# Performance work log

Hardware: AMD Instinct MI355X
Metric: run time of the kernel (lower is better)

Reference implementation:

```python
import jax, jax.numpy as jnp
import numpy as np

INPUT_DIM = 512
OUTPUT_DIM = 512
GRID_SIZE = 16
INPUT_MIN = -1.0
INPUT_RANGE = 2.0


def setup_inputs() -> dict:
    key = jax.random.key(0)
    k_x, k_mix = jax.random.split(key)
    x = jax.random.normal(k_x, (65536, INPUT_DIM), dtype=jnp.float32)
    # per-dim spline tables: bases init zeros, slopes init 0.1 (as in torch)
    bases = jnp.zeros((INPUT_DIM, GRID_SIZE), dtype=jnp.float32)
    slopes = jnp.full((INPUT_DIM, GRID_SIZE), 0.1, dtype=jnp.float32)
    mix = jax.random.normal(k_mix, (OUTPUT_DIM, INPUT_DIM), dtype=jnp.float32) * 0.01
    bias = jnp.zeros((OUTPUT_DIM,), dtype=jnp.float32)
    return {"x": x, "bases": bases, "slopes": slopes, "mix": mix, "bias": bias}


def reference(x, bases, slopes, mix, bias):
    # x: [B, D]; bases/slopes: [D, G]; mix: [O, D]; bias: [O]
    B, D = x.shape
    G = bases.shape[1]
    x_norm = jnp.clip((x - INPUT_MIN) / INPUT_RANGE, 0.0, 1.0 - 1e-6)
    idx = jnp.clip((x_norm * G).astype(jnp.int32), 0, G - 1)        # [B, D]
    x_local = x_norm * G - idx.astype(x.dtype)                       # fractional position in cell
    # gather per-dim table entries: flatten [D, G] and index with d*G + idx
    flat_idx = jnp.arange(D, dtype=jnp.int32)[None, :] * G + idx    # [B, D]
    base = bases.reshape(-1)[flat_idx]                               # [B, D]
    slope = slopes.reshape(-1)[flat_idx]                             # [B, D]
    spline_out = base + slope * x_local                              # [B, D]
    y = jnp.einsum('bd,od->bo', spline_out, mix) + bias              # [B, O]
    return y
```

## Files before the change

kernel.cpp:

```cpp
#include <hip/hip_runtime.h>


#define DIMK 512
#define DIMN 512
#define GRID_G 16

typedef unsigned short u16;
typedef unsigned int u32;
typedef __attribute__((ext_vector_type(8))) __bf16 bf16x8;
typedef __attribute__((ext_vector_type(4))) float f32x4;

__device__ __forceinline__ u32 bf16rne(float f) {
    u32 u = __float_as_uint(f);
    return (u + 0x7fffu + ((u >> 16) & 1u)) >> 16;
}

__global__ void prep_kernel(const float* __restrict__ mix,
                            u16* __restrict__ mixb) {
    int t = blockIdx.x * 256 + threadIdx.x;
    float4 v = reinterpret_cast<const float4*>(mix)[t];
    ushort4 o;
    o.x = (u16)bf16rne(v.x);
    o.y = (u16)bf16rne(v.y);
    o.z = (u16)bf16rne(v.z);
    o.w = (u16)bf16rne(v.w);
    reinterpret_cast<ushort4*>(mixb)[t] = o;
}

__global__ __launch_bounds__(512, 2) void kan_kernel(
    const float* __restrict__ x, const float* __restrict__ bases,
    const float* __restrict__ slopes, const u16* __restrict__ mixb,
    const float* __restrict__ bias, float* __restrict__ y) {
    __shared__ u32 s_tab[DIMK * 17];
    __shared__ __align__(16) u16 sA[128 * 32];
    __shared__ __align__(16) u16 sB[512 * 32];

    const int tid = threadIdx.x;
    const int lane = tid & 63;
    const int wid = tid >> 6;
    const int quad = lane >> 4;
    const int l15 = lane & 15;
    const int wave_m = wid >> 2;
    const int wave_n = wid & 3;
    const int m0 = blockIdx.x * 128;

#pragma unroll
    for (int k = 0; k < 16; k++) {
        int i = tid + k * 512;
        u32 p = bf16rne(bases[i]) | (bf16rne(slopes[i]) << 16);
        s_tab[(i >> 4) * 17 + (i & 15)] = p;
    }

    const int ar = tid >> 2;
    const int akg = tid & 3;
    const int awchunk = (ar << 2) | (akg ^ ((ar >> 1) & 3));
    const float4* xrow =
        reinterpret_cast<const float4*>(x + (size_t)(m0 + ar) * DIMK) + akg * 2;

    f32x4 acc[4][8];
#pragma unroll
    for (int i = 0; i < 4; i++)
#pragma unroll
        for (int j = 0; j < 8; j++) acc[i][j] = (f32x4){0.f, 0.f, 0.f, 0.f};

    float4 xa = xrow[0];
    float4 xb = xrow[1];

    __syncthreads();

    for (int kt = 0; kt < 16; ++kt) {
        float xs[8] = {xa.x, xa.y, xa.z, xa.w, xb.x, xb.y, xb.z, xb.w};
        const int dbase = kt * 32 + akg * 8;
        u32 h[8];
#pragma unroll
        for (int j = 0; j < 8; j++) {
            float xn = fminf(fmaxf((xs[j] + 1.0f) * 0.5f, 0.0f), 0.999999f);
            float tt = xn * 16.0f;
            int idx = (int)tt;
            u32 p = s_tab[(dbase + j) * 17 + idx];
            float base = __uint_as_float(p << 16);
            float slope = __uint_as_float(p & 0xffff0000u);
            float sp = fmaf(slope, tt - (float)idx, base);
            h[j] = bf16rne(sp);
        }
        int4 pk = make_int4((int)(h[0] | (h[1] << 16)), (int)(h[2] | (h[3] << 16)),
                            (int)(h[4] | (h[5] << 16)), (int)(h[6] | (h[7] << 16)));
        *reinterpret_cast<int4*>(&sA[awchunk * 8]) = pk;

#pragma unroll
        for (int i = 0; i < 4; i++) {
            int grp = wid * 4 + i;
            int n = grp * 16 + (lane >> 2);
            int c = (lane & 3) ^ ((n >> 1) & 3);
            const u16* gsrc = mixb + (size_t)n * DIMK + kt * 32 + c * 8;
            __builtin_amdgcn_global_load_lds(
                (const __attribute__((address_space(1))) void*)gsrc,
                (__attribute__((address_space(3))) void*)(&sB[grp * 512]),
                16, 0, 0);
        }
        __syncthreads();

        if (kt < 15) {
            xa = xrow[(kt + 1) * 8];
            xb = xrow[(kt + 1) * 8 + 1];
        }

        bf16x8 afrag[4];
#pragma unroll
        for (int fm = 0; fm < 4; fm++) {
            int m_l = wave_m * 64 + fm * 16 + l15;
            int ci = (m_l << 2) | (quad ^ ((m_l >> 1) & 3));
            afrag[fm] = *reinterpret_cast<const bf16x8*>(&sA[ci * 8]);
        }
#pragma unroll
        for (int fn = 0; fn < 8; fn++) {
            int n_l = wave_n * 128 + fn * 16 + l15;
            int ci = (n_l << 2) | (quad ^ ((n_l >> 1) & 3));
            bf16x8 bfrag = *reinterpret_cast<const bf16x8*>(&sB[ci * 8]);
#pragma unroll
            for (int fm = 0; fm < 4; fm++)
                acc[fm][fn] = __builtin_amdgcn_mfma_f32_16x16x32_bf16(
                    afrag[fm], bfrag, acc[fm][fn], 0, 0, 0);
        }
        __syncthreads();
    }

#pragma unroll
    for (int fn = 0; fn < 8; fn++) {
        int o = wave_n * 128 + fn * 16 + l15;
        float bv = bias[o];
#pragma unroll
        for (int fm = 0; fm < 4; fm++) {
            int row = m0 + wave_m * 64 + fm * 16 + quad * 4;
            float* yp = y + (size_t)row * DIMN + o;
#pragma unroll
            for (int j = 0; j < 4; j++)
                yp[(size_t)j * DIMN] = acc[fm][fn][j] + bv;
        }
    }
}

extern "C" void kernel_launch(void* const* d_in, const int* in_sizes, int n_in,
                              void* d_out, int out_size, void* d_ws, size_t ws_size,
                              hipStream_t stream) {
    const float* x = (const float*)d_in[0];
    const float* bases = (const float*)d_in[1];
    const float* slopes = (const float*)d_in[2];
    const float* mix = (const float*)d_in[3];
    const float* bias = (const float*)d_in[4];
    float* y = (float*)d_out;

    u16* mixb = (u16*)d_ws;

    hipLaunchKernelGGL(prep_kernel, dim3(256), dim3(256), 0, stream, mix, mixb);
    hipLaunchKernelGGL(kan_kernel, dim3(512), dim3(512), 0, stream,
                       x, bases, slopes, mixb, bias, y);
}
```

Before: 263.5 us.

## Split fused spline+GEMM into separate spline pass and tiled bf16 GEMM

Unfuses the kernel. A new spline kernel computes the bf16 spline activations for all of x and writes them to workspace. A separate 128x128-tiled GEMM kernel, with a 2D grid over N and 64-wide K steps, then streams both operands through global_load_lds. This frees the GEMM from per-tile spline ALU work and the large LDS table, allowing higher occupancy. The cost is an extra 64 MB intermediate write plus read, and the spline work is recomputed per N tile in neither path. It falls back to the fused kernel when the workspace is too small.

New measurement: 305.3 us. 15.9% more time.

```diff
diff --git a/kernel.cpp b/kernel.cpp
--- a/kernel.cpp
+++ b/kernel.cpp
@@ -3,7 +3,6 @@
 
 #define DIMK 512
 #define DIMN 512
-#define GRID_G 16
 
 typedef unsigned short u16;
 typedef unsigned int u32;
@@ -27,6 +26,128 @@
     reinterpret_cast<ushort4*>(mixb)[t] = o;
 }
 
+__global__ __launch_bounds__(256) void spline_kernel(
+    const float* __restrict__ x, const float* __restrict__ bases,
+    const float* __restrict__ slopes, u16* __restrict__ spl) {
+    __shared__ u32 s_tab[DIMK * 17];
+
+    const int tid = threadIdx.x;
+#pragma unroll
+    for (int k = 0; k < 32; k++) {
+        int i = tid + k * 256;
+        s_tab[(i >> 4) * 17 + (i & 15)] = bf16rne(bases[i]) | (bf16rne(slopes[i]) << 16);
+    }
+    __syncthreads();
+
+    size_t base = (size_t)blockIdx.x * 8192;
+#pragma unroll 2
+    for (int it = 0; it < 32; it++) {
+        size_t f4 = base + it * 256 + tid;
+        float4 v = reinterpret_cast<const float4*>(x)[f4];
+        int d0 = ((int)(f4 & 127)) * 4;
+        float xs[4] = {v.x, v.y, v.z, v.w};
+        u32 h[4];
+#pragma unroll
+        for (int j = 0; j < 4; j++) {
+            float xn = fminf(fmaxf((xs[j] + 1.0f) * 0.5f, 0.0f), 0.999999f);
+            float tt = xn * 16.0f;
+            int idx = (int)tt;
+            u32 p = s_tab[(d0 + j) * 17 + idx];
+            float b = __uint_as_float(p << 16);
+            float s = __uint_as_float(p & 0xffff0000u);
+            h[j] = bf16rne(fmaf(s, tt - (float)idx, b));
+        }
+        ushort4 o;
+        o.x = (u16)h[0]; o.y = (u16)h[1]; o.z = (u16)h[2]; o.w = (u16)h[3];
+        reinterpret_cast<ushort4*>(spl)[f4] = o;
+    }
+}
+
+__global__ __launch_bounds__(256, 4) void gemm_kernel(
+    const u16* __restrict__ spl, const u16* __restrict__ mixb,
+    const float* __restrict__ bias, float* __restrict__ y) {
+    __shared__ __align__(16) u16 sA[128 * 64];
+    __shared__ __align__(16) u16 sB[128 * 64];
+
+    const int tid = threadIdx.x;
+    const int lane = tid & 63;
+    const int wid = tid >> 6;
+    const int quad = lane >> 4;
+    const int l15 = lane & 15;
+    const int wave_m = wid >> 1;
+    const int wave_n = wid & 1;
+    const int m0 = blockIdx.x * 128;
+    const int n0 = blockIdx.y * 128;
+
+    f32x4 acc[4][4];
+#pragma unroll
+    for (int i = 0; i < 4; i++)
+#pragma unroll
+        for (int j = 0; j < 4; j++) acc[i][j] = (f32x4){0.f, 0.f, 0.f, 0.f};
+
+    const int grow = (lane >> 3);
+    const int gcg = (lane & 7);
+
+    for (int kt = 0; kt < 8; ++kt) {
+        const int k0 = kt * 64;
+#pragma unroll
+        for (int i = 0; i < 4; i++) {
+            int g = wid * 4 + i;
+            int row = g * 8 + grow;
+            int cg = gcg ^ (row & 7);
+            const u16* srcA = spl + (size_t)(m0 + row) * DIMK + k0 + cg * 8;
+            const u16* srcB = mixb + (size_t)(n0 + row) * DIMK + k0 + cg * 8;
+            __builtin_amdgcn_global_load_lds(
+                (const __attribute__((address_space(1))) void*)srcA,
+                (__attribute__((address_space(3))) void*)((char*)sA + g * 1024),
+                16, 0, 0);
+            __builtin_amdgcn_global_load_lds(
+                (const __attribute__((address_space(1))) void*)srcB,
+                (__attribute__((address_space(3))) void*)((char*)sB + g * 1024),
+                16, 0, 0);
+        }
+        __syncthreads();
+
+#pragma unroll
+        for (int ks = 0; ks < 2; ks++) {
+            bf16x8 af[4], bf[4];
+#pragma unroll
+            for (int fm = 0; fm < 4; fm++) {
+                int row = wave_m * 64 + fm * 16 + l15;
+                int c = ((ks << 2) | quad) ^ (row & 7);
+                af[fm] = *reinterpret_cast<const bf16x8*>(&sA[row * 64 + c * 8]);
+            }
+#pragma unroll
+            for (int fn = 0; fn < 4; fn++) {
+                int row = wave_n * 64 + fn * 16 + l15;
+                int c = ((ks << 2) | quad) ^ (row & 7);
+                bf[fn] = *reinterpret_cast<const bf16x8*>(&sB[row * 64 + c * 8]);
+            }
+#pragma unroll
+            for (int fn = 0; fn < 4; fn++)
+#pragma unroll
+                for (int fm = 0; fm < 4; fm++)
+                    acc[fm][fn] = __builtin_amdgcn_mfma_f32_16x16x32_bf16(
+                        af[fm], bf[fn], acc[fm][fn], 0, 0, 0);
+        }
+        __syncthreads();
+    }
+
+#pragma unroll
+    for (int fn = 0; fn < 4; fn++) {
+        int o = n0 + wave_n * 64 + fn * 16 + l15;
+        float bv = bias[o];
+#pragma unroll
+        for (int fm = 0; fm < 4; fm++) {
+            int r0 = m0 + wave_m * 64 + fm * 16 + quad * 4;
+            float* yp = y + (size_t)r0 * DIMN + o;
+#pragma unroll
+            for (int j = 0; j < 4; j++)
+                yp[(size_t)j * DIMN] = acc[fm][fn][j] + bv;
+        }
+    }
+}
+
 __global__ __launch_bounds__(512, 2) void kan_kernel(
     const float* __restrict__ x, const float* __restrict__ bases,
     const float* __restrict__ slopes, const u16* __restrict__ mixb,
@@ -47,8 +168,7 @@
 #pragma unroll
     for (int k = 0; k < 16; k++) {
         int i = tid + k * 512;
-        u32 p = bf16rne(bases[i]) | (bf16rne(slopes[i]) << 16);
-        s_tab[(i >> 4) * 17 + (i & 15)] = p;
+        s_tab[(i >> 4) * 17 + (i & 15)] = bf16rne(bases[i]) | (bf16rne(slopes[i]) << 16);
     }
 
     const int ar = tid >> 2;
@@ -65,7 +185,6 @@
 
     float4 xa = xrow[0];
     float4 xb = xrow[1];
-
     __syncthreads();
 
     for (int kt = 0; kt < 16; ++kt) {
@@ -80,8 +199,7 @@
             u32 p = s_tab[(dbase + j) * 17 + idx];
             float base = __uint_as_float(p << 16);
             float slope = __uint_as_float(p & 0xffff0000u);
-            float sp = fmaf(slope, tt - (float)idx, base);
-            h[j] = bf16rne(sp);
+            h[j] = bf16rne(fmaf(slope, tt - (float)idx, base));
         }
         int4 pk = make_int4((int)(h[0] | (h[1] << 16)), (int)(h[2] | (h[3] << 16)),
                             (int)(h[4] | (h[5] << 16)), (int)(h[6] | (h[7] << 16)));
@@ -151,8 +269,18 @@
     float* y = (float*)d_out;
 
     u16* mixb = (u16*)d_ws;
+    const size_t need = 512 * 1024 + (size_t)65536 * 512 * 2;
 
     hipLaunchKernelGGL(prep_kernel, dim3(256), dim3(256), 0, stream, mix, mixb);
-    hipLaunchKernelGGL(kan_kernel, dim3(512), dim3(512), 0, stream,
-                       x, bases, slopes, mixb, bias, y);
-}
+
+    if (ws_size >= need) {
+        u16* spl = (u16*)((char*)d_ws + 512 * 1024);
+        hipLaunchKernelGGL(spline_kernel, dim3(1024), dim3(256), 0, stream,
+                           x, bases, slopes, spl);
+        hipLaunchKernelGGL(gemm_kernel, dim3(512, 4), dim3(256), 0, stream,
+                           spl, mixb, bias, y);
+    } else {
+        hipLaunchKernelGGL(kan_kernel, dim3(512), dim3(512), 0, stream,
+                           x, bases, slopes, mixb, bias, y);
+    }
+}
```
